# Kernel tuning notes

Measured on AMD Instinct MI355X. Metric: run time of the kernel, lower is better.

## Reference

```python
import jax, jax.numpy as jnp
import numpy as np

ALPHA = 0.2  # LeakyReLU negative slope
NEG_BIG = -9e15

def setup_inputs() -> dict:
    key = jax.random.key(0)
    k1, k2, k3, k4 = jax.random.split(key, 4)
    N, F_IN, F_OUT = 8192, 128, 128
    h = jax.random.normal(k1, (N, F_IN), dtype=jnp.float32)
    adj = jax.random.randint(k2, (N, N), 0, 2, dtype=jnp.int32)
    # xavier-uniform-ish params
    W = jax.random.normal(k3, (F_IN, F_OUT), dtype=jnp.float32) * (1.0 / np.sqrt(F_IN))
    a = jax.random.normal(k4, (2 * F_OUT, 1), dtype=jnp.float32) * (1.0 / np.sqrt(2 * F_OUT))
    return {"h": h, "adj": adj, "W": W, "a": a}

def reference(h, adj, W, a):
    # Wh: [N, F_OUT]
    Wh = h @ W
    F_out = Wh.shape[1]
    # a_input @ a == (Wh @ a1)_i + (Wh @ a2)_j  (same math, no N^2*2F tensor)
    a1 = a[:F_out, 0]   # [F_OUT]
    a2 = a[F_out:, 0]   # [F_OUT]
    e = (Wh @ a1)[:, None] + (Wh @ a2)[None, :]        # [N, N]
    e = jnp.where(e >= 0, e, ALPHA * e)                # LeakyReLU(0.2)
    scores = jnp.where(adj > 0, e, NEG_BIG)
    attention = jax.nn.softmax(scores, axis=1)         # row-wise
    # dropout skipped (eval mode / training=False)
    return attention @ Wh                              # [N, F_OUT]
```

## Files before the change

### kernel.cpp

```cpp
#include <hip/hip_runtime.h>
#include <hip/hip_bf16.h>

#define N 8192
#define FD 128
#define LOG2E 1.4426950408889634f

typedef __attribute__((ext_vector_type(4))) float f4;
typedef __attribute__((ext_vector_type(4))) int i32x4;
typedef __attribute__((ext_vector_type(4))) unsigned int u32x4;
typedef __attribute__((ext_vector_type(8))) __bf16 bf16x8;

__device__ __forceinline__ unsigned short bfbits(float x){
  __bf16 b = (__bf16)x;
  return __builtin_bit_cast(unsigned short, b);
}

__global__ __launch_bounds__(256) void k12_wh(const float* __restrict__ h,
                                              const float* __restrict__ W,
                                              const float* __restrict__ a,
                                              unsigned short* __restrict__ Bsw,
                                              float* __restrict__ s1L,
                                              float* __restrict__ s2L){
  __shared__ float Wl[64*128];
  __shared__ float hT[128*33];
  int t = threadIdx.x;
  int i0 = blockIdx.x * 32;
  {
    int r  = t >> 3;
    int k0 = (t & 7) * 16;
    const f4* src = (const f4*)&h[(size_t)(i0 + r)*FD + k0];
    #pragma unroll
    for (int q = 0; q < 4; ++q){
      f4 v = src[q];
      #pragma unroll
      for (int e = 0; e < 4; ++e) hT[(k0 + q*4 + e)*33 + r] = v[e];
    }
  }
  int f0 = (t & 31) * 4;
  int r0 = (t >> 5) * 4;
  float acc[4][4] = {};
  for (int half = 0; half < 2; ++half){
    __syncthreads();
    #pragma unroll
    for (int v = 0; v < 8; ++v){
      int idx = (v*256 + t)*4;
      *(f4*)&Wl[idx] = *(const f4*)&W[half*8192 + idx];
    }
    __syncthreads();
    for (int k2 = 0; k2 < 64; ++k2){
      f4 wv = *(const f4*)&Wl[k2*FD + f0];
      f4 hv = *(const f4*)&hT[(half*64 + k2)*33 + r0];
      #pragma unroll
      for (int ri = 0; ri < 4; ++ri)
        #pragma unroll
        for (int fi = 0; fi < 4; ++fi)
          acc[ri][fi] = __builtin_fmaf(hv[ri], wv[fi], acc[ri][fi]);
    }
  }
  int jblk = blockIdx.x;
  int n  = f0 >> 4;
  int fl = f0 & 15;
  #pragma unroll
  for (int ri = 0; ri < 4; ++ri){
    int k = r0 + ri;
    size_t base = (((size_t)jblk*8 + n)*64 + ((k>>3)<<4))*8 + (k&7);
    #pragma unroll
    for (int fi = 0; fi < 4; ++fi)
      Bsw[base + (size_t)(fl + fi)*8] = bfbits(acc[ri][fi]);
  }
  f4 a1v = *(const f4*)&a[f0];
  f4 a2v = *(const f4*)&a[FD + f0];
  float p1[4], p2[4];
  #pragma unroll
  for (int ri = 0; ri < 4; ++ri){
    p1[ri] = 0.f; p2[ri] = 0.f;
    #pragma unroll
    for (int fi = 0; fi < 4; ++fi){
      p1[ri] = __builtin_fmaf(acc[ri][fi], a1v[fi], p1[ri]);
      p2[ri] = __builtin_fmaf(acc[ri][fi], a2v[fi], p2[ri]);
    }
  }
  #pragma unroll
  for (int d = 1; d < 32; d <<= 1){
    #pragma unroll
    for (int ri = 0; ri < 4; ++ri){
      p1[ri] += __shfl_xor(p1[ri], d, 32);
      p2[ri] += __shfl_xor(p2[ri], d, 32);
    }
  }
  if ((t & 31) == 0){
    #pragma unroll
    for (int ri = 0; ri < 4; ++ri){
      s1L[i0 + r0 + ri] = p1[ri] * LOG2E;
      s2L[i0 + r0 + ri] = p2[ri] * LOG2E;
    }
  }
}

__global__ __launch_bounds__(256) void k3_max(const float* __restrict__ s2L,
                                              float* __restrict__ M2L){
  __shared__ float red[4];
  int t = threadIdx.x;
  float m = -3.0e38f;
  for (int i = t; i < N; i += 256) m = fmaxf(m, s2L[i]);
  #pragma unroll
  for (int d = 1; d < 64; d <<= 1) m = fmaxf(m, __shfl_xor(m, d, 64));
  if ((t & 63) == 0) red[t >> 6] = m;
  __syncthreads();
  if (t == 0) *M2L = fmaxf(fmaxf(red[0], red[1]), fmaxf(red[2], red[3]));
}

__global__ __launch_bounds__(256,2) void k4_flash(const int* __restrict__ adj,
    const unsigned short* __restrict__ Bsw,
    const float* __restrict__ s1L, const float* __restrict__ s2L,
    const float* __restrict__ M2p,
    float* __restrict__ partial, float* __restrict__ denomp, int njc){
  __shared__ unsigned char mk[4][2][16][32];
  int t = threadIdx.x;
  int wv = t >> 6, lane = t & 63;
  int lrow = lane & 15, lgrp = lane >> 4;
  int i0w = blockIdx.x * 64 + wv * 16;
  int jlen = N / njc;
  int jstart = blockIdx.y * jlen;
  int nmac = jlen >> 8;
  float M2 = *M2p;
  float s1a = s1L[i0w + lrow];
  float ea = s1a + M2;
  float maL = fmaxf(ea, 0.2f*ea);

  f4 acc[8];
  #pragma unroll
  for (int n = 0; n < 8; ++n) acc[n] = (f4){0.f,0.f,0.f,0.f};
  f4 accd = (f4){0.f,0.f,0.f,0.f};
  u32x4 onesbits = (u32x4){0x3F803F80u,0x3F803F80u,0x3F803F80u,0x3F803F80u};
  bf16x8 ones = __builtin_bit_cast(bf16x8, onesbits);

  const i32x4* adj4 = (const i32x4*)adj;
  const f4* s2v = (const f4*)s2L;
  size_t stbase = (((size_t)(i0w + (lane >> 5)) * N) + (size_t)(lane & 31) * 8) >> 2;
  const size_t rowstep2 = ((size_t)2 * N) >> 2;

  i32x4 st[16];
  {
    size_t b0 = stbase + ((size_t)jstart >> 2);
    #pragma unroll
    for (int p = 0; p < 8; ++p){
      st[2*p]   = adj4[b0 + (size_t)p * rowstep2];
      st[2*p+1] = adj4[b0 + (size_t)p * rowstep2 + 1];
    }
    #pragma unroll
    for (int p = 0; p < 8; ++p){
      unsigned v = 0;
      #pragma unroll
      for (int e = 0; e < 4; ++e){
        v |= (st[2*p][e]   != 0) ? (1u << e)     : 0u;
        v |= (st[2*p+1][e] != 0) ? (1u << (4+e)) : 0u;
      }
      mk[wv][0][2*p + (lane >> 5)][lane & 31] = (unsigned char)v;
    }
  }

  for (int m = 0; m < nmac; ++m){
    int bf = m & 1;
    int jbase = jstart + m*256;
    if (m + 1 < nmac){
      size_t bn = stbase + ((size_t)(jbase + 256) >> 2);
      #pragma unroll
      for (int p = 0; p < 8; ++p){
        st[2*p]   = adj4[bn + (size_t)p * rowstep2];
        st[2*p+1] = adj4[bn + (size_t)p * rowstep2 + 1];
      }
    }
    int jt0 = jbase >> 5;
    #pragma unroll
    for (int js = 0; js < 8; ++js){
      int jb = jbase + js*32 + lgrp*8;
      unsigned mbyte = mk[wv][bf][lrow][js*4 + lgrp];
      f4 ya = s2v[jb >> 2], yb = s2v[(jb >> 2) + 1];
      u32x4 braw[8];
      #pragma unroll
      for (int n = 0; n < 8; ++n)
        braw[n] = *(const u32x4*)&Bsw[((((size_t)(jt0 + js)*8 + n)*64) + lane)*8];
      bf16x8 fa;
      #pragma unroll
      for (int e = 0; e < 8; ++e){
        float sj = (e < 4) ? ya[e] : yb[e-4];
        float x  = s1a + sj;
        float lr = fmaxf(x, 0.2f*x);
        float p  = ((mbyte >> e) & 1u) ? __builtin_amdgcn_exp2f(lr - maL) : 0.f;
        fa[e] = (__bf16)p;
      }
      accd = __builtin_amdgcn_mfma_f32_16x16x32_bf16(fa, ones, accd, 0, 0, 0);
      #pragma unroll
      for (int n = 0; n < 8; ++n)
        acc[n] = __builtin_amdgcn_mfma_f32_16x16x32_bf16(fa,
                   __builtin_bit_cast(bf16x8, braw[n]), acc[n], 0, 0, 0);
    }
    if (m + 1 < nmac){
      #pragma unroll
      for (int p = 0; p < 8; ++p){
        unsigned v = 0;
        #pragma unroll
        for (int e = 0; e < 4; ++e){
          v |= (st[2*p][e]   != 0) ? (1u << e)     : 0u;
          v |= (st[2*p+1][e] != 0) ? (1u << (4+e)) : 0u;
        }
        mk[wv][bf ^ 1][2*p + (lane >> 5)][lane & 31] = (unsigned char)v;
      }
    }
  }

  if (lrow == 0){
    #pragma unroll
    for (int r = 0; r < 4; ++r)
      denomp[(size_t)blockIdx.y*N + i0w + lgrp*4 + r] = accd[r];
  }
  float* pb = partial + (size_t)blockIdx.y * N * FD;
  #pragma unroll
  for (int n = 0; n < 8; ++n)
    #pragma unroll
    for (int r = 0; r < 4; ++r)
      pb[(size_t)(i0w + lgrp*4 + r)*FD + n*16 + lrow] = acc[n][r];
}

__global__ __launch_bounds__(256) void k5_fin(const float* __restrict__ partial,
    const float* __restrict__ denomp, float* __restrict__ out, int njc){
  int g = blockIdx.x*256 + threadIdx.x;
  int i = g >> 7;
  float num = 0.f, den = 0.f;
  for (int c = 0; c < njc; ++c) num += partial[(size_t)c*N*FD + g];
  for (int c = 0; c < njc; ++c) den += denomp[(size_t)c*N + i];
  out[g] = num / den;
}

extern "C" void kernel_launch(void* const* d_in, const int* in_sizes, int n_in,
                              void* d_out, int out_size, void* d_ws, size_t ws_size,
                              hipStream_t stream){
  const float* h   = (const float*)d_in[0];
  const int*   adj = (const int*)d_in[1];
  const float* W   = (const float*)d_in[2];
  const float* a   = (const float*)d_in[3];
  float* out = (float*)d_out;
  char* ws = (char*)d_ws;

  unsigned short* Bsw = (unsigned short*)ws;
  float* s1L = (float*)(ws + (size_t)(6u<<20));
  float* s2L = (float*)(ws + (size_t)(6u<<20) + 32768);
  float* M2L = (float*)(ws + (size_t)(6u<<20) + 65536);
  float* denomp  = (float*)(ws + (size_t)(7u<<20));
  float* partial = (float*)(ws + (size_t)(8u<<20));

  size_t chunk = (size_t)N * FD * sizeof(float);
  int njc = 1;
  if (ws_size > ((size_t)(8u<<20))){
    size_t m = (ws_size - (size_t)(8u<<20)) / chunk;
    njc = (m >= 8) ? 8 : (m >= 4) ? 4 : (m >= 2) ? 2 : 1;
  }

  hipLaunchKernelGGL(k12_wh, dim3(256), dim3(256), 0, stream, h, W, a, Bsw, s1L, s2L);
  hipLaunchKernelGGL(k3_max, dim3(1),   dim3(256), 0, stream, s2L, M2L);
  hipLaunchKernelGGL(k4_flash, dim3(128, njc), dim3(256), 0, stream,
                     adj, Bsw, s1L, s2L, M2L, partial, denomp, njc);
  hipLaunchKernelGGL(k5_fin, dim3(N*FD/256), dim3(256), 0, stream, partial, denomp, out, njc);
}
```

Baseline: 486.3 us.

## Stage Wh tiles in LDS and give each wave two row tiles

After: 448.2 us. 7.8% less time.

```diff
diff --git a/kernel.cpp b/kernel.cpp
--- a/kernel.cpp
+++ b/kernel.cpp
@@ -115,112 +115,109 @@
     const float* __restrict__ s1L, const float* __restrict__ s2L,
     const float* __restrict__ M2p,
     float* __restrict__ partial, float* __restrict__ denomp, int njc){
-  __shared__ unsigned char mk[4][2][16][32];
+  __shared__ unsigned char bswl[32768];
+  __shared__ unsigned long long mkl[128][2];
+  __shared__ float s2l[128];
   int t = threadIdx.x;
   int wv = t >> 6, lane = t & 63;
   int lrow = lane & 15, lgrp = lane >> 4;
-  int i0w = blockIdx.x * 64 + wv * 16;
+  int bx = blockIdx.x;
   int jlen = N / njc;
   int jstart = blockIdx.y * jlen;
-  int nmac = jlen >> 8;
+  int nmac = jlen >> 7;
   float M2 = *M2p;
-  float s1a = s1L[i0w + lrow];
-  float ea = s1a + M2;
+  int i0w = bx*128 + wv*32;
+  float s1a = s1L[i0w + lrow], s1b = s1L[i0w + 16 + lrow];
+  float ea = s1a + M2, eb = s1b + M2;
   float maL = fmaxf(ea, 0.2f*ea);
-
-  f4 acc[8];
-  #pragma unroll
-  for (int n = 0; n < 8; ++n) acc[n] = (f4){0.f,0.f,0.f,0.f};
-  f4 accd = (f4){0.f,0.f,0.f,0.f};
+  float mbL = fmaxf(eb, 0.2f*eb);
+
+  f4 acc[2][8]; f4 accd[2];
+  #pragma unroll
+  for (int x = 0; x < 2; ++x){
+    accd[x] = (f4){0.f,0.f,0.f,0.f};
+    #pragma unroll
+    for (int n = 0; n < 8; ++n) acc[x][n] = (f4){0.f,0.f,0.f,0.f};
+  }
   u32x4 onesbits = (u32x4){0x3F803F80u,0x3F803F80u,0x3F803F80u,0x3F803F80u};
   bf16x8 ones = __builtin_bit_cast(bf16x8, onesbits);
 
-  const i32x4* adj4 = (const i32x4*)adj;
-  const f4* s2v = (const f4*)s2L;
-  size_t stbase = (((size_t)(i0w + (lane >> 5)) * N) + (size_t)(lane & 31) * 8) >> 2;
-  const size_t rowstep2 = ((size_t)2 * N) >> 2;
-
-  i32x4 st[16];
-  {
-    size_t b0 = stbase + ((size_t)jstart >> 2);
-    #pragma unroll
-    for (int p = 0; p < 8; ++p){
-      st[2*p]   = adj4[b0 + (size_t)p * rowstep2];
-      st[2*p+1] = adj4[b0 + (size_t)p * rowstep2 + 1];
-    }
-    #pragma unroll
-    for (int p = 0; p < 8; ++p){
-      unsigned v = 0;
-      #pragma unroll
-      for (int e = 0; e < 4; ++e){
-        v |= (st[2*p][e]   != 0) ? (1u << e)     : 0u;
-        v |= (st[2*p+1][e] != 0) ? (1u << (4+e)) : 0u;
-      }
-      mk[wv][0][2*p + (lane >> 5)][lane & 31] = (unsigned char)v;
-    }
-  }
+  int srow = t >> 1;
+  int shalf = t & 1;
+  const i32x4* adjrow = (const i32x4*)(adj + (size_t)(bx*128 + srow)*N);
 
   for (int m = 0; m < nmac; ++m){
-    int bf = m & 1;
-    int jbase = jstart + m*256;
-    if (m + 1 < nmac){
-      size_t bn = stbase + ((size_t)(jbase + 256) >> 2);
-      #pragma unroll
-      for (int p = 0; p < 8; ++p){
-        st[2*p]   = adj4[bn + (size_t)p * rowstep2];
-        st[2*p+1] = adj4[bn + (size_t)p * rowstep2 + 1];
-      }
-    }
-    int jt0 = jbase >> 5;
-    #pragma unroll
-    for (int js = 0; js < 8; ++js){
-      int jb = jbase + js*32 + lgrp*8;
-      unsigned mbyte = mk[wv][bf][lrow][js*4 + lgrp];
-      f4 ya = s2v[jb >> 2], yb = s2v[(jb >> 2) + 1];
+    int jb0 = jstart + m*128;
+    i32x4 st[16];
+    int ib = (jb0 + shalf*64) >> 2;
+    #pragma unroll
+    for (int e = 0; e < 16; ++e) st[e] = adjrow[ib + e];
+    {
+      const u32x4* src = (const u32x4*)(Bsw + (size_t)(jb0 >> 5) * 4096);
+      u32x4* dst = (u32x4*)bswl;
+      #pragma unroll
+      for (int q = 0; q < 8; ++q)
+        dst[q*256 + t] = src[q*256 + t];
+    }
+    if (t < 128) s2l[t] = s2L[jb0 + t];
+    unsigned long long mv = 0ull;
+    #pragma unroll
+    for (int e = 0; e < 16; ++e){
+      #pragma unroll
+      for (int c = 0; c < 4; ++c)
+        mv |= (st[e][c] != 0) ? (1ull << (e*4 + c)) : 0ull;
+    }
+    mkl[srow][shalf] = mv;
+    __syncthreads();
+    const unsigned char* mkb = (const unsigned char*)mkl;
+    #pragma unroll
+    for (int js = 0; js < 4; ++js){
+      int jo = js*32 + lgrp*8;
+      f4 ya = *(const f4*)&s2l[jo];
+      f4 yb = *(const f4*)&s2l[jo+4];
+      unsigned mba = mkb[(wv*32 + lrow)*16 + js*4 + lgrp];
+      unsigned mbb = mkb[(wv*32 + 16 + lrow)*16 + js*4 + lgrp];
       u32x4 braw[8];
       #pragma unroll
       for (int n = 0; n < 8; ++n)
-        braw[n] = *(const u32x4*)&Bsw[((((size_t)(jt0 + js)*8 + n)*64) + lane)*8];
-      bf16x8 fa;
+        braw[n] = *(const u32x4*)&bswl[((js*8 + n)*64 + lane)*16];
+      bf16x8 fa, fb;
       #pragma unroll
       for (int e = 0; e < 8; ++e){
         float sj = (e < 4) ? ya[e] : yb[e-4];
-        float x  = s1a + sj;
-        float lr = fmaxf(x, 0.2f*x);
-        float p  = ((mbyte >> e) & 1u) ? __builtin_amdgcn_exp2f(lr - maL) : 0.f;
-        fa[e] = (__bf16)p;
+        float xa = s1a + sj,               xb = s1b + sj;
+        float la = fmaxf(xa, 0.2f*xa),     lb = fmaxf(xb, 0.2f*xb);
+        float pa = ((mba>>e)&1u) ? __builtin_amdgcn_exp2f(la - maL) : 0.f;
+        float pb = ((mbb>>e)&1u) ? __builtin_amdgcn_exp2f(lb - mbL) : 0.f;
+        fa[e] = (__bf16)pa; fb[e] = (__bf16)pb;
       }
-      accd = __builtin_amdgcn_mfma_f32_16x16x32_bf16(fa, ones, accd, 0, 0, 0);
-      #pragma unroll
-      for (int n = 0; n < 8; ++n)
-        acc[n] = __builtin_amdgcn_mfma_f32_16x16x32_bf16(fa,
-                   __builtin_bit_cast(bf16x8, braw[n]), acc[n], 0, 0, 0);
-    }
-    if (m + 1 < nmac){
-      #pragma unroll
-      for (int p = 0; p < 8; ++p){
-        unsigned v = 0;
-        #pragma unroll
-        for (int e = 0; e < 4; ++e){
-          v |= (st[2*p][e]   != 0) ? (1u << e)     : 0u;
-          v |= (st[2*p+1][e] != 0) ? (1u << (4+e)) : 0u;
-        }
-        mk[wv][bf ^ 1][2*p + (lane >> 5)][lane & 31] = (unsigned char)v;
+      accd[0] = __builtin_amdgcn_mfma_f32_16x16x32_bf16(fa, ones, accd[0], 0, 0, 0);
+      accd[1] = __builtin_amdgcn_mfma_f32_16x16x32_bf16(fb, ones, accd[1], 0, 0, 0);
+      #pragma unroll
+      for (int n = 0; n < 8; ++n){
+        bf16x8 bb = __builtin_bit_cast(bf16x8, braw[n]);
+        acc[0][n] = __builtin_amdgcn_mfma_f32_16x16x32_bf16(fa, bb, acc[0][n], 0, 0, 0);
+        acc[1][n] = __builtin_amdgcn_mfma_f32_16x16x32_bf16(fb, bb, acc[1][n], 0, 0, 0);
       }
     }
+    __syncthreads();
   }
 
   if (lrow == 0){
     #pragma unroll
-    for (int r = 0; r < 4; ++r)
-      denomp[(size_t)blockIdx.y*N + i0w + lgrp*4 + r] = accd[r];
+    for (int x = 0; x < 2; ++x)
+      #pragma unroll
+      for (int r = 0; r < 4; ++r)
+        denomp[(size_t)blockIdx.y*N + i0w + x*16 + lgrp*4 + r] = accd[x][r];
   }
   float* pb = partial + (size_t)blockIdx.y * N * FD;
   #pragma unroll
-  for (int n = 0; n < 8; ++n)
-    #pragma unroll
-    for (int r = 0; r < 4; ++r)
-      pb[(size_t)(i0w + lgrp*4 + r)*FD + n*16 + lrow] = acc[n][r];
+  for (int x = 0; x < 2; ++x)
+    #pragma unroll
+    for (int n = 0; n < 8; ++n)
+      #pragma unroll
+      for (int r = 0; r < 4; ++r)
+        pb[(size_t)(i0w + x*16 + lgrp*4 + r)*FD + n*16 + lrow] = acc[x][n][r];
 }
 
 __global__ __launch_bounds__(256) void k5_fin(const float* __restrict__ partial,
@@ -259,7 +256,7 @@
 
   hipLaunchKernelGGL(k12_wh, dim3(256), dim3(256), 0, stream, h, W, a, Bsw, s1L, s2L);
   hipLaunchKernelGGL(k3_max, dim3(1),   dim3(256), 0, stream, s2L, M2L);
-  hipLaunchKernelGGL(k4_flash, dim3(128, njc), dim3(256), 0, stream,
+  hipLaunchKernelGGL(k4_flash, dim3(64, njc), dim3(256), 0, stream,
                      adj, Bsw, s1L, s2L, M2L, partial, denomp, njc);
   hipLaunchKernelGGL(k5_fin, dim3(N*FD/256), dim3(256), 0, stream, partial, denomp, out, njc);
 }
```

## Precompress adjacency into bitmask kernel and stage mask/scores in LDS for flash kernel

Applied to the files above, without the earlier changes.

Measured after the change: 474.2 us. -2.5%, faster.

```diff
diff --git a/kernel.cpp b/kernel.cpp
--- a/kernel.cpp
+++ b/kernel.cpp
@@ -4,6 +4,7 @@
 #define N 8192
 #define FD 128
 #define LOG2E 1.4426950408889634f
+#define CMSTR 132
 
 typedef __attribute__((ext_vector_type(4))) float f4;
 typedef __attribute__((ext_vector_type(4))) int i32x4;
@@ -13,6 +14,21 @@
 __device__ __forceinline__ unsigned short bfbits(float x){
   __bf16 b = (__bf16)x;
   return __builtin_bit_cast(unsigned short, b);
+}
+
+__global__ __launch_bounds__(256) void kc_compress(const int* __restrict__ adj,
+                                                   unsigned char* __restrict__ cmask){
+  int tid = blockIdx.x*256 + threadIdx.x;
+  const int TOT = 2048*256;
+  const i32x4* adj4 = (const i32x4*)adj;
+  #pragma unroll 4
+  for (int k = 0; k < 16; ++k){
+    size_t g = (size_t)tid + (size_t)k*TOT;
+    i32x4 a = adj4[g*2], b = adj4[g*2+1];
+    unsigned v = (a[0]!=0?1u:0u) | (a[1]!=0?2u:0u) | (a[2]!=0?4u:0u) | (a[3]!=0?8u:0u)
+               | (b[0]!=0?16u:0u)| (b[1]!=0?32u:0u)| (b[2]!=0?64u:0u)| (b[3]!=0?128u:0u);
+    cmask[g] = (unsigned char)v;
+  }
 }
 
 __global__ __launch_bounds__(256) void k12_wh(const float* __restrict__ h,
@@ -110,85 +126,64 @@
   if (t == 0) *M2L = fmaxf(fmaxf(red[0], red[1]), fmaxf(red[2], red[3]));
 }
 
-__global__ __launch_bounds__(256,2) void k4_flash(const int* __restrict__ adj,
+__global__ __launch_bounds__(256,4) void k4_flash(const unsigned char* __restrict__ cmask,
     const unsigned short* __restrict__ Bsw,
     const float* __restrict__ s1L, const float* __restrict__ s2L,
     const float* __restrict__ M2p,
     float* __restrict__ partial, float* __restrict__ denomp, int njc){
-  __shared__ unsigned char mk[4][2][16][32];
+  __shared__ __align__(16) unsigned char cml[64*CMSTR];
+  __shared__ __align__(16) float s2l[1024];
   int t = threadIdx.x;
   int wv = t >> 6, lane = t & 63;
   int lrow = lane & 15, lgrp = lane >> 4;
-  int i0w = blockIdx.x * 64 + wv * 16;
-  int jlen = N / njc;
-  int jstart = blockIdx.y * jlen;
-  int nmac = jlen >> 8;
+  int bid = blockIdx.x;
+  int y  = bid & 7;
+  int bx = bid >> 3;
+  int jstart = y * 1024;
   float M2 = *M2p;
+  int i0w = bx*64 + wv*16;
   float s1a = s1L[i0w + lrow];
   float ea = s1a + M2;
   float maL = fmaxf(ea, 0.2f*ea);
 
-  f4 acc[8];
+  {
+    int rr = t >> 2, sg = (t & 3) * 32;
+    const unsigned char* src = cmask + (size_t)(bx*64 + rr)*(N/8) + (jstart >> 3) + sg;
+    *(u32x4*)&cml[rr*CMSTR + sg]      = *(const u32x4*)(src);
+    *(u32x4*)&cml[rr*CMSTR + sg + 16] = *(const u32x4*)(src + 16);
+  }
+  *(f4*)&s2l[t*4] = *(const f4*)&s2L[jstart + t*4];
+  __syncthreads();
+
+  f4 acc[8]; f4 accd = (f4){0.f,0.f,0.f,0.f};
   #pragma unroll
   for (int n = 0; n < 8; ++n) acc[n] = (f4){0.f,0.f,0.f,0.f};
-  f4 accd = (f4){0.f,0.f,0.f,0.f};
   u32x4 onesbits = (u32x4){0x3F803F80u,0x3F803F80u,0x3F803F80u,0x3F803F80u};
   bf16x8 ones = __builtin_bit_cast(bf16x8, onesbits);
 
-  const i32x4* adj4 = (const i32x4*)adj;
-  const f4* s2v = (const f4*)s2L;
-  size_t stbase = (((size_t)(i0w + (lane >> 5)) * N) + (size_t)(lane & 31) * 8) >> 2;
-  const size_t rowstep2 = ((size_t)2 * N) >> 2;
-
-  i32x4 st[16];
-  {
-    size_t b0 = stbase + ((size_t)jstart >> 2);
-    #pragma unroll
-    for (int p = 0; p < 8; ++p){
-      st[2*p]   = adj4[b0 + (size_t)p * rowstep2];
-      st[2*p+1] = adj4[b0 + (size_t)p * rowstep2 + 1];
-    }
-    #pragma unroll
-    for (int p = 0; p < 8; ++p){
-      unsigned v = 0;
-      #pragma unroll
-      for (int e = 0; e < 4; ++e){
-        v |= (st[2*p][e]   != 0) ? (1u << e)     : 0u;
-        v |= (st[2*p+1][e] != 0) ? (1u << (4+e)) : 0u;
-      }
-      mk[wv][0][2*p + (lane >> 5)][lane & 31] = (unsigned char)v;
-    }
-  }
-
-  for (int m = 0; m < nmac; ++m){
-    int bf = m & 1;
-    int jbase = jstart + m*256;
-    if (m + 1 < nmac){
-      size_t bn = stbase + ((size_t)(jbase + 256) >> 2);
-      #pragma unroll
-      for (int p = 0; p < 8; ++p){
-        st[2*p]   = adj4[bn + (size_t)p * rowstep2];
-        st[2*p+1] = adj4[bn + (size_t)p * rowstep2 + 1];
-      }
-    }
-    int jt0 = jbase >> 5;
-    #pragma unroll
-    for (int js = 0; js < 8; ++js){
-      int jb = jbase + js*32 + lgrp*8;
-      unsigned mbyte = mk[wv][bf][lrow][js*4 + lgrp];
-      f4 ya = s2v[jb >> 2], yb = s2v[(jb >> 2) + 1];
+  int rA = (wv*16 + lrow)*CMSTR;
+  int jt0 = jstart >> 5;
+
+  for (int m = 0; m < 16; ++m){
+    #pragma unroll
+    for (int js = 0; js < 2; ++js){
+      int jt = jt0 + m*2 + js;
+      int jo = m*64 + js*32 + lgrp*8;
       u32x4 braw[8];
       #pragma unroll
       for (int n = 0; n < 8; ++n)
-        braw[n] = *(const u32x4*)&Bsw[((((size_t)(jt0 + js)*8 + n)*64) + lane)*8];
+        braw[n] = *(const u32x4*)&Bsw[(((size_t)jt*8 + n)*64 + lane)*8];
+      f4 ya = *(const f4*)&s2l[jo];
+      f4 yb = *(const f4*)&s2l[jo+4];
+      unsigned mba = cml[rA + m*8 + js*4 + lgrp];
       bf16x8 fa;
       #pragma unroll
       for (int e = 0; e < 8; ++e){
-        float sj = (e < 4) ? ya[e] : yb[e-4];
-        float x  = s1a + sj;
-        float lr = fmaxf(x, 0.2f*x);
-        float p  = ((mbyte >> e) & 1u) ? __builtin_amdgcn_exp2f(lr - maL) : 0.f;
-        fa[e] = (__bf16)p;
+        float sjv = (e < 4) ? ya[e] : yb[e-4];
+        float xa = s1a + sjv;
+        float la = fmaxf(xa, 0.2f*xa);
+        float pa = ((mba>>e)&1u) ? __builtin_amdgcn_exp2f(la - maL) : 0.f;
+        fa[e] = (__bf16)pa;
       }
       accd = __builtin_amdgcn_mfma_f32_16x16x32_bf16(fa, ones, accd, 0, 0, 0);
       #pragma unroll
@@ -196,26 +191,14 @@
         acc[n] = __builtin_amdgcn_mfma_f32_16x16x32_bf16(fa,
                    __builtin_bit_cast(bf16x8, braw[n]), acc[n], 0, 0, 0);
     }
-    if (m + 1 < nmac){
-      #pragma unroll
-      for (int p = 0; p < 8; ++p){
-        unsigned v = 0;
-        #pragma unroll
-        for (int e = 0; e < 4; ++e){
-          v |= (st[2*p][e]   != 0) ? (1u << e)     : 0u;
-          v |= (st[2*p+1][e] != 0) ? (1u << (4+e)) : 0u;
-        }
-        mk[wv][bf ^ 1][2*p + (lane >> 5)][lane & 31] = (unsigned char)v;
-      }
-    }
   }
 
   if (lrow == 0){
     #pragma unroll
     for (int r = 0; r < 4; ++r)
-      denomp[(size_t)blockIdx.y*N + i0w + lgrp*4 + r] = accd[r];
-  }
-  float* pb = partial + (size_t)blockIdx.y * N * FD;
+      denomp[(size_t)y*N + i0w + lgrp*4 + r] = accd[r];
+  }
+  float* pb = partial + (size_t)y * N * FD;
   #pragma unroll
   for (int n = 0; n < 8; ++n)
     #pragma unroll
@@ -249,17 +232,14 @@
   float* M2L = (float*)(ws + (size_t)(6u<<20) + 65536);
   float* denomp  = (float*)(ws + (size_t)(7u<<20));
   float* partial = (float*)(ws + (size_t)(8u<<20));
-
-  size_t chunk = (size_t)N * FD * sizeof(float);
-  int njc = 1;
-  if (ws_size > ((size_t)(8u<<20))){
-    size_t m = (ws_size - (size_t)(8u<<20)) / chunk;
-    njc = (m >= 8) ? 8 : (m >= 4) ? 4 : (m >= 2) ? 2 : 1;
-  }
-
+  unsigned char* cmask = (unsigned char*)(ws + (size_t)(40u<<20));
+
+  const int njc = 8;
+
+  hipLaunchKernelGGL(kc_compress, dim3(2048), dim3(256), 0, stream, adj, cmask);
   hipLaunchKernelGGL(k12_wh, dim3(256), dim3(256), 0, stream, h, W, a, Bsw, s1L, s2L);
   hipLaunchKernelGGL(k3_max, dim3(1),   dim3(256), 0, stream, s2L, M2L);
-  hipLaunchKernelGGL(k4_flash, dim3(128, njc), dim3(256), 0, stream,
-                     adj, Bsw, s1L, s2L, M2L, partial, denomp, njc);
+  hipLaunchKernelGGL(k4_flash, dim3(128*njc), dim3(256), 0, stream,
+                     cmask, Bsw, s1L, s2L, M2L, partial, denomp, njc);
   hipLaunchKernelGGL(k5_fin, dim3(N*FD/256), dim3(256), 0, stream, partial, denomp, out, njc);
 }
```
